# Performance work log

Measured on AMD Instinct MI355X. Metric: run time of the kernel, lower is better.

## Reference

```python
import jax, jax.numpy as jnp
import numpy as np

B, S, HID = 4, 1024, 1024
H, HK, D = 16, 8, 64
EPS = 1e-6
THETA = 10000.0
ROPE_SCALE = 1.0


def _rms_norm(x, gamma=None):
    # RMSNorm over head_dim; Gemma-style (1+gamma) scale, v_norm has no scale.
    v = x * jax.lax.rsqrt(jnp.mean(x * x, axis=-1, keepdims=True) + EPS)
    return v if gamma is None else v * (1.0 + gamma)


def _rope_1d(x, pos, theta, scale):
    # x: [B,S,h,d], pos: [B,S] -> rotate-half RoPE along d
    d = x.shape[-1]
    inv_freq = 1.0 / (theta ** (jnp.arange(0, d, 2, dtype=jnp.float32) / d))  # [d/2]
    ang = (pos.astype(jnp.float32) / scale)[..., None] * inv_freq             # [B,S,d/2]
    cos = jnp.cos(ang)[:, :, None, :]
    sin = jnp.sin(ang)[:, :, None, :]
    x1, x2 = x[..., : d // 2], x[..., d // 2 :]
    return jnp.concatenate([x1 * cos - x2 * sin, x2 * cos + x1 * sin], axis=-1)


def _multidim_rope(x, positions_xy, theta, scale):
    # split head_dim in half: first half rotated by x-position, second by y-position
    d = x.shape[-1]
    xh, yh = x[..., : d // 2], x[..., d // 2 :]
    return jnp.concatenate(
        [_rope_1d(xh, positions_xy[..., 0], theta, scale),
         _rope_1d(yh, positions_xy[..., 1], theta, scale)], axis=-1)


def setup_inputs() -> dict:
    key = jax.random.key(0)
    ks = jax.random.split(key, 8)
    std = 0.02
    return {
        "hidden_states": jax.random.normal(ks[0], (B, S, HID), jnp.float32),
        "Wq": jax.random.normal(ks[1], (HID, H * D), jnp.float32) * std,
        "Wk": jax.random.normal(ks[2], (HID, HK * D), jnp.float32) * std,
        "Wv": jax.random.normal(ks[3], (HID, HK * D), jnp.float32) * std,
        "Wo": jax.random.normal(ks[4], (H * D, HID), jnp.float32) * std,
        "q_gamma": jax.random.normal(ks[5], (D,), jnp.float32) * 0.02,
        "k_gamma": jax.random.normal(ks[6], (D,), jnp.float32) * 0.02,
        "positions_xy": jax.random.randint(ks[7], (B, S, 2), 0, 32, dtype=jnp.int32),
        "attention_mask": jnp.ones((B, S, S), dtype=bool),
    }


def reference(hidden_states, Wq, Wk, Wv, Wo, q_gamma, k_gamma, positions_xy, attention_mask):
    b, s, _ = hidden_states.shape
    q = (hidden_states @ Wq).reshape(b, s, H, D)
    k = (hidden_states @ Wk).reshape(b, s, HK, D)
    v = (hidden_states @ Wv).reshape(b, s, HK, D)
    q = _rms_norm(q, q_gamma)
    k = _rms_norm(k, k_gamma)
    v = _rms_norm(v)  # no scale
    q = _multidim_rope(q, positions_xy, THETA, ROPE_SCALE).transpose(0, 2, 1, 3)  # [B,H,S,D]
    k = _multidim_rope(k, positions_xy, THETA, ROPE_SCALE).transpose(0, 2, 1, 3)  # [B,HK,S,D]
    v = v.transpose(0, 2, 1, 3)                                                   # [B,HK,S,D]
    groups = H // HK
    k = jnp.repeat(k, groups, axis=1)  # GQA expand -> [B,H,S,D]
    v = jnp.repeat(v, groups, axis=1)
    # scale=1.0 per the original SDPA call (no 1/sqrt(d))
    logits = jnp.einsum("bhqd,bhkd->bhqk", q, k)
    neg = jnp.asarray(jnp.finfo(logits.dtype).min, logits.dtype)
    logits = jnp.where(attention_mask[:, None, :, :], logits, neg)
    probs = jax.nn.softmax(logits.astype(jnp.float32), axis=-1).astype(q.dtype)
    out = jnp.einsum("bhqk,bhkd->bhqd", probs, v)
    out = out.transpose(0, 2, 1, 3).reshape(b, s, H * D)
    return out @ Wo
```

## Files before the change

kernel.cpp:

```cpp
#include <hip/hip_runtime.h>
#include <hip/hip_bf16.h>
#include <stdint.h>

typedef __attribute__((ext_vector_type(8))) short short8;
typedef __attribute__((ext_vector_type(4))) float f32x4;

#define MFMA16(a, b, c) __builtin_amdgcn_mfma_f32_16x16x32_bf16(a, b, c, 0, 0, 0)

__device__ __forceinline__ unsigned short f2bf_u(float f) {
  union { float f; uint32_t u; } x; x.f = f;
  uint32_t r = (x.u + 0x7fffu + ((x.u >> 16) & 1u)) >> 16;
  return (unsigned short)r;
}
__device__ __forceinline__ short f2bf(float f) { return (short)f2bf_u(f); }

__device__ __forceinline__ uint32_t pack_bf2(float lo, float hi) {
  __hip_bfloat162 h = __float22bfloat162_rn(make_float2(lo, hi));
  union { __hip_bfloat162 h; uint32_t u; } c; c.h = h;
  return c.u;
}

__device__ __forceinline__ void gload_lds16(const void* g, void* lds) {
  __builtin_amdgcn_global_load_lds(
      (const __attribute__((address_space(1))) uint32_t*)(uintptr_t)g,
      (__attribute__((address_space(3))) uint32_t*)(uintptr_t)lds,
      16, 0, 0);
}

__global__ __launch_bounds__(256) void convert_bf16_kernel(
    const float* __restrict__ in, short* __restrict__ out, int n4) {
  int i = blockIdx.x * 256 + threadIdx.x;
  if (i >= n4) return;
  float4 v = reinterpret_cast<const float4*>(in)[i];
  short4 o;
  o.x = f2bf(v.x); o.y = f2bf(v.y); o.z = f2bf(v.z); o.w = f2bf(v.w);
  reinterpret_cast<short4*>(out)[i] = o;
}

__global__ __launch_bounds__(256) void transpose_all_kernel(
    const float* __restrict__ Wq, const float* __restrict__ Wk,
    const float* __restrict__ Wv, const float* __restrict__ Wo,
    short* __restrict__ WTQKV, short* __restrict__ WOT) {
  __shared__ float tile[32][33];
  int yb = blockIdx.y;
  const float* src; short* dst; int N; int yy;
  if (yb < 32)      { src = Wq; dst = WTQKV;                       N = 1024; yy = yb; }
  else if (yb < 48) { src = Wk; dst = WTQKV + (size_t)1024 * 1024; N = 512;  yy = yb - 32; }
  else if (yb < 64) { src = Wv; dst = WTQKV + (size_t)1536 * 1024; N = 512;  yy = yb - 48; }
  else              { src = Wo; dst = WOT;                         N = 1024; yy = yb - 64; }
  int k0 = blockIdx.x * 32, n0 = yy * 32;
  int tx = threadIdx.x, ty = threadIdx.y;
#pragma unroll
  for (int i = 0; i < 4; ++i)
    tile[ty + 8 * i][tx] = src[(size_t)(k0 + ty + 8 * i) * N + n0 + tx];
  __syncthreads();
#pragma unroll
  for (int i = 0; i < 4; ++i)
    dst[(size_t)(n0 + ty + 8 * i) * 1024 + k0 + tx] = f2bf(tile[tx][ty + 8 * i]);
}

__global__ __launch_bounds__(256) void gemm_qkv_fused(
    const short* __restrict__ A, const short* __restrict__ BT,
    const float* __restrict__ qg, const float* __restrict__ kg,
    const int* __restrict__ pos,
    short* __restrict__ Qp, short* __restrict__ Kp, short* __restrict__ Vt) {
  const int K = 1024;
  __shared__ short As[2 * 128 * 32];
  __shared__ short Bs[2 * 128 * 32];
  int wg = blockIdx.x + gridDim.x * blockIdx.y;
  int lid = (wg & 7) * 64 + (wg >> 3);
  int m0 = (lid & 31) * 128, n0 = (lid >> 5) * 128;
  int t = threadIdx.x;
  int w = t >> 6, lane = t & 63;
  int wr = w >> 1, wc = w & 1;
  int lr = lane & 15, lg = lane >> 4;

  f32x4 acc[4][4] = {};

  for (int k0 = 0; k0 < K; k0 += 64) {
    __syncthreads();
#pragma unroll
    for (int i = 0; i < 4; ++i) {
      int q = t + 256 * i;
      int kk = q >> 9, row = (q >> 2) & 127, c = q & 3;
      gload_lds16(A + (size_t)(m0 + row) * K + k0 + kk * 32 + c * 8, &As[q * 8]);
      gload_lds16(BT + (size_t)(n0 + row) * K + k0 + kk * 32 + c * 8, &Bs[q * 8]);
    }
    __syncthreads();
#pragma unroll
    for (int kk = 0; kk < 2; ++kk) {
      short8 af[4], bf[4];
#pragma unroll
      for (int mi = 0; mi < 4; ++mi)
        af[mi] = *(const short8*)&As[kk * 4096 + (wr * 64 + mi * 16 + lr) * 32 + lg * 8];
#pragma unroll
      for (int ni = 0; ni < 4; ++ni)
        bf[ni] = *(const short8*)&Bs[kk * 4096 + (wc * 64 + ni * 16 + lr) * 32 + lg * 8];
      __builtin_amdgcn_s_setprio(1);
#pragma unroll
      for (int mi = 0; mi < 4; ++mi)
#pragma unroll
        for (int ni = 0; ni < 4; ++ni)
          acc[mi][ni] = MFMA16(af[mi], bf[ni], acc[mi][ni]);
      __builtin_amdgcn_s_setprio(0);
    }
  }

  int g = (n0 >> 6) + wc;
  int row0 = m0 + wr * 64;
  const int2* posv = (const int2*)pos;

  if (g < 24) {
    const float* gsrc = (g < 16) ? qg : kg;
    short* dst = (g < 16) ? Qp : Kp;
    int nh = (g < 16) ? 16 : 8;
    int h = (g < 16) ? g : g - 16;
    float gscale = (g < 16) ? 1.4426950408889634f : 1.0f;
    float gam[4];
#pragma unroll
    for (int ni = 0; ni < 4; ++ni) gam[ni] = (1.0f + gsrc[ni * 16 + lr]) * gscale;
    float invf = exp2f((float)lr * -0.8304820237218405f);
#pragma unroll
    for (int mi = 0; mi < 4; ++mi) {
      f32x4 ss = acc[mi][0] * acc[mi][0];
#pragma unroll
      for (int ni = 1; ni < 4; ++ni) ss += acc[mi][ni] * acc[mi][ni];
#pragma unroll
      for (int m2 = 1; m2 < 16; m2 <<= 1)
#pragma unroll
        for (int r = 0; r < 4; ++r) ss[r] += __shfl_xor(ss[r], m2);
#pragma unroll
      for (int r = 0; r < 4; ++r) {
        int row = row0 + mi * 16 + lg * 4 + r;
        float inv = rsqrtf(ss[r] * 0.015625f + 1e-6f);
        float v0 = acc[mi][0][r] * inv * gam[0];
        float v1 = acc[mi][1][r] * inv * gam[1];
        float v2 = acc[mi][2][r] * inv * gam[2];
        float v3 = acc[mi][3][r] * inv * gam[3];
        int2 pp = posv[row];
        float sx, cx, sy, cy;
        __sincosf((float)pp.x * invf, &sx, &cx);
        __sincosf((float)pp.y * invf, &sy, &cy);
        float o0 = v0 * cx - v1 * sx, o1 = v1 * cx + v0 * sx;
        float o2 = v2 * cy - v3 * sy, o3 = v3 * cy + v2 * sy;
        int s = row & 1023, bb = row >> 10;
        short* base = dst + ((size_t)((bb * nh + h) * 1024 + s)) * 64;
        base[lr]      = f2bf(o0);
        base[lr + 16] = f2bf(o1);
        base[lr + 32] = f2bf(o2);
        base[lr + 48] = f2bf(o3);
      }
    }
  } else {
    int hk = g - 24;
#pragma unroll
    for (int mi = 0; mi < 4; ++mi) {
      f32x4 ss = acc[mi][0] * acc[mi][0];
#pragma unroll
      for (int ni = 1; ni < 4; ++ni) ss += acc[mi][ni] * acc[mi][ni];
#pragma unroll
      for (int m2 = 1; m2 < 16; m2 <<= 1)
#pragma unroll
        for (int r = 0; r < 4; ++r) ss[r] += __shfl_xor(ss[r], m2);
      f32x4 inv;
#pragma unroll
      for (int r = 0; r < 4; ++r) inv[r] = rsqrtf(ss[r] * 0.015625f + 1e-6f);
      int row = row0 + mi * 16 + lg * 4;
      int s0 = row & 1023, bb = row >> 10;
#pragma unroll
      for (int ni = 0; ni < 4; ++ni) {
        short4 sv;
        sv.x = f2bf(acc[mi][ni][0] * inv[0]);
        sv.y = f2bf(acc[mi][ni][1] * inv[1]);
        sv.z = f2bf(acc[mi][ni][2] * inv[2]);
        sv.w = f2bf(acc[mi][ni][3] * inv[3]);
        int d = ni * 16 + lr;
        *(short4*)&Vt[((size_t)((bb * 8 + hk) * 64 + d)) * 1024 + s0] = sv;
      }
    }
  }
}

__global__ __launch_bounds__(256) void gemm_bf16_bn64(
    const short* __restrict__ A, const short* __restrict__ BT,
    float* __restrict__ C, int M, int N, int K) {
  __shared__ short As[2 * 128 * 32];
  __shared__ short Bs[2 * 64 * 32];
  int wg = blockIdx.x + gridDim.x * blockIdx.y;
  int lid = (wg & 7) * 64 + (wg >> 3);
  int m0 = (lid & 31) * 128, n0 = (lid >> 5) * 64;
  int t = threadIdx.x;
  int w = t >> 6, lane = t & 63;
  int lr = lane & 15, lg = lane >> 4;

  f32x4 acc[2][4] = {};

  for (int k0 = 0; k0 < K; k0 += 64) {
    __syncthreads();
#pragma unroll
    for (int i = 0; i < 4; ++i) {
      int q = t + 256 * i;
      int kk = q >> 9, row = (q >> 2) & 127, c = q & 3;
      gload_lds16(A + (size_t)(m0 + row) * K + k0 + kk * 32 + c * 8, &As[q * 8]);
    }
#pragma unroll
    for (int i = 0; i < 2; ++i) {
      int q = t + 256 * i;
      int kk = q >> 8, row = (q >> 2) & 63, c = q & 3;
      gload_lds16(BT + (size_t)(n0 + row) * K + k0 + kk * 32 + c * 8, &Bs[q * 8]);
    }
    __syncthreads();
#pragma unroll
    for (int kk = 0; kk < 2; ++kk) {
      short8 af[2], bf[4];
#pragma unroll
      for (int mi = 0; mi < 2; ++mi)
        af[mi] = *(const short8*)&As[kk * 4096 + (w * 32 + mi * 16 + lr) * 32 + lg * 8];
#pragma unroll
      for (int ni = 0; ni < 4; ++ni)
        bf[ni] = *(const short8*)&Bs[kk * 2048 + (ni * 16 + lr) * 32 + lg * 8];
      __builtin_amdgcn_s_setprio(1);
#pragma unroll
      for (int mi = 0; mi < 2; ++mi)
#pragma unroll
        for (int ni = 0; ni < 4; ++ni)
          acc[mi][ni] = MFMA16(af[mi], bf[ni], acc[mi][ni]);
      __builtin_amdgcn_s_setprio(0);
    }
  }
#pragma unroll
  for (int mi = 0; mi < 2; ++mi)
#pragma unroll
    for (int ni = 0; ni < 4; ++ni) {
      int row = m0 + w * 32 + mi * 16 + lg * 4;
      int col = n0 + ni * 16 + lr;
#pragma unroll
      for (int r = 0; r < 4; ++r)
        C[(size_t)(row + r) * N + col] = acc[mi][ni][r];
    }
}

__global__ __launch_bounds__(256) void attn_kernel(
    const short* __restrict__ Qp, const short* __restrict__ Kp,
    const short* __restrict__ Vt, short* __restrict__ attn) {
  __shared__ short Ks[2][4096];
  __shared__ short Vs[2][4096];
  __shared__ uint32_t Pl[4][16 * 20];
  int wg = blockIdx.x;
  int xcd = wg & 7, slot = wg >> 3;
  int group = xcd * 8 + (slot >> 4);
  int qb = slot & 15;
  int b = group >> 4, h = group & 15;
  int hk = h >> 1;
  int t = threadIdx.x;
  int w = t >> 6, lane = t & 63;
  int lr = lane & 15, lg = lane >> 4;
  int q0 = qb * 64 + w * 16;

  const short* Qb = Qp + ((size_t)(b * 16 + h) * 1024) * 64;
  const short* Kb = Kp + ((size_t)(b * 8 + hk) * 1024) * 64;
  const short* Vb = Vt + ((size_t)(b * 8 + hk) * 64) * 1024;

  short8 qf[2];
#pragma unroll
  for (int f = 0; f < 2; ++f)
    qf[f] = *(const short8*)&Qb[(q0 + lr) * 64 + f * 32 + lg * 8];

  f32x4 acc[4] = {};
  float lsum = 0.0f;
  int co = (lg ^ ((lr >> 1) & 3)) * 8;
  uint32_t* pw = &Pl[w][0];

  auto STAGE = [&](short* ksb, short* vsb, int kt) {
    int kv0 = kt * 64;
#pragma unroll
    for (int i = 0; i < 2; ++i) {
      int q = t + 256 * i;
      int f = q >> 8, rem = q & 255, kv = rem >> 2, cslot = rem & 3;
      int csrc = cslot ^ ((kv >> 1) & 3);
      gload_lds16(Kb + (size_t)(kv0 + kv) * 64 + f * 32 + csrc * 8, &ksb[q * 8]);
    }
#pragma unroll
    for (int i = 0; i < 2; ++i) {
      int q = t + 256 * i;
      int kvs = q >> 8, rem = q & 255, d = rem >> 2, cslot = rem & 3;
      int csrc = cslot ^ ((d >> 1) & 3);
      gload_lds16(Vb + (size_t)d * 1024 + kv0 + kvs * 32 + csrc * 8, &vsb[q * 8]);
    }
  };

  auto COMPUTE = [&](const short* ksb, const short* vsb) {
    f32x4 sv[4];
    __builtin_amdgcn_s_setprio(1);
#pragma unroll
    for (int kvb = 0; kvb < 4; ++kvb) {
      int ro = (kvb * 16 + lr) * 32 + co;
      short8 a0 = *(const short8*)&ksb[ro];
      short8 a1 = *(const short8*)&ksb[2048 + ro];
      f32x4 s = {};
      s = MFMA16(a0, qf[0], s);
      s = MFMA16(a1, qf[1], s);
      sv[kvb] = s;
    }
    __builtin_amdgcn_s_setprio(0);
    uint32_t pk[4][2];
#pragma unroll
    for (int kvb = 0; kvb < 4; ++kvb) {
      float p0 = exp2f(sv[kvb][0]), p1 = exp2f(sv[kvb][1]);
      float p2 = exp2f(sv[kvb][2]), p3 = exp2f(sv[kvb][3]);
      lsum += (p0 + p1) + (p2 + p3);
      pk[kvb][0] = pack_bf2(p0, p1);
      pk[kvb][1] = pack_bf2(p2, p3);
    }
#pragma unroll
    for (int kvs = 0; kvs < 2; ++kvs) {
      *(uint2*)&pw[lr * 20 + 2 * lg]     = make_uint2(pk[kvs * 2][0], pk[kvs * 2][1]);
      *(uint2*)&pw[lr * 20 + 8 + 2 * lg] = make_uint2(pk[kvs * 2 + 1][0], pk[kvs * 2 + 1][1]);
      short8 pb = *(const short8*)&pw[lr * 20 + 4 * lg];
      __builtin_amdgcn_s_setprio(1);
#pragma unroll
      for (int db = 0; db < 4; ++db) {
        short8 vf = *(const short8*)&vsb[kvs * 2048 + (db * 16 + lr) * 32 + co];
        acc[db] = MFMA16(vf, pb, acc[db]);
      }
      __builtin_amdgcn_s_setprio(0);
    }
  };

  STAGE(Ks[0], Vs[0], 0);
  __syncthreads();
  int cur = 0;
  for (int kt = 0; kt < 15; ++kt) {
    STAGE(Ks[cur ^ 1], Vs[cur ^ 1], kt + 1);
    __builtin_amdgcn_sched_barrier(0);
    COMPUTE(Ks[cur], Vs[cur]);
    __syncthreads();
    cur ^= 1;
  }
  COMPUTE(Ks[cur], Vs[cur]);

  lsum += __shfl_xor(lsum, 16);
  lsum += __shfl_xor(lsum, 32);
  float inv = 1.0f / lsum;
  size_t rowbase = ((size_t)(b * 1024 + q0 + lr)) * 1024 + h * 64;
#pragma unroll
  for (int db = 0; db < 4; ++db) {
    uint32_t w0 = pack_bf2(acc[db][0] * inv, acc[db][1] * inv);
    uint32_t w1 = pack_bf2(acc[db][2] * inv, acc[db][3] * inv);
    uint32_t* pp = (uint32_t*)&attn[rowbase + db * 16 + lg * 4];
    pp[0] = w0;
    pp[1] = w1;
  }
}

extern "C" void kernel_launch(void* const* d_in, const int* in_sizes, int n_in,
                              void* d_out, int out_size, void* d_ws, size_t ws_size,
                              hipStream_t stream) {
  const float* X  = (const float*)d_in[0];
  const float* Wq = (const float*)d_in[1];
  const float* Wk = (const float*)d_in[2];
  const float* Wv = (const float*)d_in[3];
  const float* Wo = (const float*)d_in[4];
  const float* qg = (const float*)d_in[5];
  const float* kg = (const float*)d_in[6];
  const int* pos  = (const int*)d_in[7];
  float* out = (float*)d_out;

  char* ws = (char*)d_ws;
  short* XB    = (short*)(ws);
  short* WTQKV = (short*)(ws + ((size_t)8 << 20));
  short* WOT   = (short*)(ws + ((size_t)12 << 20));
  short* QP    = (short*)(ws + ((size_t)14 << 20));
  short* KP    = (short*)(ws + ((size_t)22 << 20));
  short* VT    = (short*)(ws + ((size_t)26 << 20));
  short* ATT   = (short*)(ws + ((size_t)30 << 20));

  convert_bf16_kernel<<<4096, 256, 0, stream>>>(X, XB, 1048576);
  transpose_all_kernel<<<dim3(32, 96), dim3(32, 8), 0, stream>>>(Wq, Wk, Wv, Wo, WTQKV, WOT);

  gemm_qkv_fused<<<dim3(32, 16), 256, 0, stream>>>(XB, WTQKV, qg, kg, pos, QP, KP, VT);
  attn_kernel<<<1024, 256, 0, stream>>>(QP, KP, VT, ATT);
  gemm_bf16_bn64<<<dim3(32, 16), 256, 0, stream>>>(ATT, WOT, out, 4096, 1024, 1024);
}
```

Baseline: 102.6 us.

## Switch attention to 32x32x16 MFMA with register-resident P and 128-row blocks

```diff
diff --git a/kernel.cpp b/kernel.cpp
--- a/kernel.cpp
+++ b/kernel.cpp
@@ -3,9 +3,12 @@
 #include <stdint.h>
 
 typedef __attribute__((ext_vector_type(8))) short short8;
+typedef __attribute__((ext_vector_type(4))) short s16x4;
 typedef __attribute__((ext_vector_type(4))) float f32x4;
+typedef __attribute__((ext_vector_type(16))) float f32x16;
 
 #define MFMA16(a, b, c) __builtin_amdgcn_mfma_f32_16x16x32_bf16(a, b, c, 0, 0, 0)
+#define MFMA32(a, b, c) __builtin_amdgcn_mfma_f32_32x32x16_bf16(a, b, c, 0, 0, 0)
 
 __device__ __forceinline__ unsigned short f2bf_u(float f) {
   union { float f; uint32_t u; } x; x.f = f;
@@ -245,85 +248,85 @@
     const short* __restrict__ Vt, short* __restrict__ attn) {
   __shared__ short Ks[2][4096];
   __shared__ short Vs[2][4096];
-  __shared__ uint32_t Pl[4][16 * 20];
   int wg = blockIdx.x;
   int xcd = wg & 7, slot = wg >> 3;
-  int group = xcd * 8 + (slot >> 4);
-  int qb = slot & 15;
+  int group = xcd * 8 + (slot >> 3);
+  int qblk = slot & 7;
   int b = group >> 4, h = group & 15;
   int hk = h >> 1;
   int t = threadIdx.x;
   int w = t >> 6, lane = t & 63;
-  int lr = lane & 15, lg = lane >> 4;
-  int q0 = qb * 64 + w * 16;
+  int l31 = lane & 31, hh = lane >> 5;
+  int xr = l31 & 7;
+  int q0 = qblk * 128 + w * 32;
 
   const short* Qb = Qp + ((size_t)(b * 16 + h) * 1024) * 64;
   const short* Kb = Kp + ((size_t)(b * 8 + hk) * 1024) * 64;
   const short* Vb = Vt + ((size_t)(b * 8 + hk) * 64) * 1024;
 
-  short8 qf[2];
-#pragma unroll
-  for (int f = 0; f < 2; ++f)
-    qf[f] = *(const short8*)&Qb[(q0 + lr) * 64 + f * 32 + lg * 8];
-
-  f32x4 acc[4] = {};
-  float lsum = 0.0f;
-  int co = (lg ^ ((lr >> 1) & 3)) * 8;
-  uint32_t* pw = &Pl[w][0];
+  short8 qf[4];
+#pragma unroll
+  for (int dk = 0; dk < 4; ++dk)
+    qf[dk] = *(const short8*)&Qb[(q0 + l31) * 64 + dk * 16 + hh * 8];
+
+  f32x16 acc[2] = {};
+  f32x4 lsumv = {};
 
   auto STAGE = [&](short* ksb, short* vsb, int kt) {
     int kv0 = kt * 64;
 #pragma unroll
     for (int i = 0; i < 2; ++i) {
       int q = t + 256 * i;
-      int f = q >> 8, rem = q & 255, kv = rem >> 2, cslot = rem & 3;
-      int csrc = cslot ^ ((kv >> 1) & 3);
-      gload_lds16(Kb + (size_t)(kv0 + kv) * 64 + f * 32 + csrc * 8, &ksb[q * 8]);
+      int kv = q >> 3, cd = q & 7, cs = cd ^ (kv & 7);
+      gload_lds16(Kb + (size_t)(kv0 + kv) * 64 + cs * 8, &ksb[q * 8]);
     }
 #pragma unroll
     for (int i = 0; i < 2; ++i) {
       int q = t + 256 * i;
-      int kvs = q >> 8, rem = q & 255, d = rem >> 2, cslot = rem & 3;
-      int csrc = cslot ^ ((d >> 1) & 3);
-      gload_lds16(Vb + (size_t)d * 1024 + kv0 + kvs * 32 + csrc * 8, &vsb[q * 8]);
+      int d = q >> 3, cd = q & 7, cs = cd ^ (d & 7);
+      gload_lds16(Vb + (size_t)d * 1024 + kv0 + cs * 8, &vsb[q * 8]);
     }
   };
 
   auto COMPUTE = [&](const short* ksb, const short* vsb) {
-    f32x4 sv[4];
-    __builtin_amdgcn_s_setprio(1);
-#pragma unroll
-    for (int kvb = 0; kvb < 4; ++kvb) {
-      int ro = (kvb * 16 + lr) * 32 + co;
-      short8 a0 = *(const short8*)&ksb[ro];
-      short8 a1 = *(const short8*)&ksb[2048 + ro];
-      f32x4 s = {};
-      s = MFMA16(a0, qf[0], s);
-      s = MFMA16(a1, qf[1], s);
-      sv[kvb] = s;
-    }
-    __builtin_amdgcn_s_setprio(0);
-    uint32_t pk[4][2];
-#pragma unroll
-    for (int kvb = 0; kvb < 4; ++kvb) {
-      float p0 = exp2f(sv[kvb][0]), p1 = exp2f(sv[kvb][1]);
-      float p2 = exp2f(sv[kvb][2]), p3 = exp2f(sv[kvb][3]);
-      lsum += (p0 + p1) + (p2 + p3);
-      pk[kvb][0] = pack_bf2(p0, p1);
-      pk[kvb][1] = pack_bf2(p2, p3);
-    }
-#pragma unroll
-    for (int kvs = 0; kvs < 2; ++kvs) {
-      *(uint2*)&pw[lr * 20 + 2 * lg]     = make_uint2(pk[kvs * 2][0], pk[kvs * 2][1]);
-      *(uint2*)&pw[lr * 20 + 8 + 2 * lg] = make_uint2(pk[kvs * 2 + 1][0], pk[kvs * 2 + 1][1]);
-      short8 pb = *(const short8*)&pw[lr * 20 + 4 * lg];
+#pragma unroll
+    for (int kvb2 = 0; kvb2 < 2; ++kvb2) {
+      f32x16 sv = {};
       __builtin_amdgcn_s_setprio(1);
 #pragma unroll
-      for (int db = 0; db < 4; ++db) {
-        short8 vf = *(const short8*)&vsb[kvs * 2048 + (db * 16 + lr) * 32 + co];
-        acc[db] = MFMA16(vf, pb, acc[db]);
+      for (int dk = 0; dk < 4; ++dk) {
+        short8 kf = *(const short8*)&ksb[(kvb2 * 32 + l31) * 64 + ((dk * 2 + hh) ^ xr) * 8];
+        sv = MFMA32(kf, qf[dk], sv);
       }
       __builtin_amdgcn_s_setprio(0);
+      float p[16];
+#pragma unroll
+      for (int r = 0; r < 16; ++r) p[r] = exp2f(sv[r]);
+#pragma unroll
+      for (int r = 0; r < 16; r += 4) {
+        lsumv[0] += p[r]; lsumv[1] += p[r + 1];
+        lsumv[2] += p[r + 2]; lsumv[3] += p[r + 3];
+      }
+      uint32_t pk8[8];
+#pragma unroll
+      for (int j = 0; j < 8; ++j) pk8[j] = pack_bf2(p[2 * j], p[2 * j + 1]);
+#pragma unroll
+      for (int kvc = 0; kvc < 2; ++kvc) {
+        union { uint32_t u[4]; short8 s; } pb;
+#pragma unroll
+        for (int j = 0; j < 4; ++j) pb.u[j] = pk8[kvc * 4 + j];
+        int cg = kvb2 * 4 + kvc * 2;
+        __builtin_amdgcn_s_setprio(1);
+#pragma unroll
+        for (int db2 = 0; db2 < 2; ++db2) {
+          int dd = db2 * 32 + l31;
+          union { s16x4 h4[2]; short8 s; } vu;
+          vu.h4[0] = *(const s16x4*)&vsb[dd * 64 + ((cg ^ xr) * 8) + 4 * hh];
+          vu.h4[1] = *(const s16x4*)&vsb[dd * 64 + (((cg + 1) ^ xr) * 8) + 4 * hh];
+          acc[db2] = MFMA32(vu.s, pb.s, acc[db2]);
+        }
+        __builtin_amdgcn_s_setprio(0);
+      }
     }
   };
 
@@ -339,18 +342,19 @@
   }
   COMPUTE(Ks[cur], Vs[cur]);
 
-  lsum += __shfl_xor(lsum, 16);
+  float lsum = (lsumv[0] + lsumv[1]) + (lsumv[2] + lsumv[3]);
   lsum += __shfl_xor(lsum, 32);
   float inv = 1.0f / lsum;
-  size_t rowbase = ((size_t)(b * 1024 + q0 + lr)) * 1024 + h * 64;
-#pragma unroll
-  for (int db = 0; db < 4; ++db) {
-    uint32_t w0 = pack_bf2(acc[db][0] * inv, acc[db][1] * inv);
-    uint32_t w1 = pack_bf2(acc[db][2] * inv, acc[db][3] * inv);
-    uint32_t* pp = (uint32_t*)&attn[rowbase + db * 16 + lg * 4];
-    pp[0] = w0;
-    pp[1] = w1;
-  }
+  short* orow = attn + ((size_t)(b * 1024 + q0 + l31)) * 1024 + h * 64;
+#pragma unroll
+  for (int db2 = 0; db2 < 2; ++db2)
+#pragma unroll
+    for (int g2 = 0; g2 < 4; ++g2) {
+      int d0 = db2 * 32 + g2 * 8 + 4 * hh;
+      uint32_t w0 = pack_bf2(acc[db2][g2 * 4 + 0] * inv, acc[db2][g2 * 4 + 1] * inv);
+      uint32_t w1 = pack_bf2(acc[db2][g2 * 4 + 2] * inv, acc[db2][g2 * 4 + 3] * inv);
+      *(uint2*)&orow[d0] = make_uint2(w0, w1);
+    }
 }
 
 extern "C" void kernel_launch(void* const* d_in, const int* in_sizes, int n_in,
@@ -379,6 +383,6 @@
   transpose_all_kernel<<<dim3(32, 96), dim3(32, 8), 0, stream>>>(Wq, Wk, Wv, Wo, WTQKV, WOT);
 
   gemm_qkv_fused<<<dim3(32, 16), 256, 0, stream>>>(XB, WTQKV, qg, kg, pos, QP, KP, VT);
-  attn_kernel<<<1024, 256, 0, stream>>>(QP, KP, VT, ATT);
+  attn_kernel<<<512, 256, 0, stream>>>(QP, KP, VT, ATT);
   gemm_bf16_bn64<<<dim3(32, 16), 256, 0, stream>>>(ATT, WOT, out, 4096, 1024, 1024);
 }
```

After: 100.8 us. Within noise of the previous version (-1.7%).
